# Performance work log

Hardware: AMD Instinct MI355X
Metric: run time of the kernel (lower is better)

## Reference

```python
import jax, jax.numpy as jnp
import numpy as np

D_MODEL = 1024
N_HEADS = 16
D_HEAD = D_MODEL // N_HEADS
D_FF = 4096
EPS = 1e-5


def _layernorm(x, g, b):
    mu = jnp.mean(x, axis=-1, keepdims=True)
    var = jnp.mean(jnp.square(x - mu), axis=-1, keepdims=True)
    return (x - mu) * jax.lax.rsqrt(var + EPS) * g + b


def setup_inputs() -> dict:
    key = jax.random.key(0)
    ks = jax.random.split(key, 16)
    B, S, D = 2, 2048, D_MODEL

    def xavier(k, shape):
        fan_in, fan_out = shape[0], shape[1]
        lim = float(np.sqrt(6.0 / (fan_in + fan_out)))
        return jax.random.uniform(k, shape, jnp.float32, -lim, lim)

    return {
        "x": jax.random.normal(ks[0], (B, S, D), jnp.float32),
        "ln1_g": jnp.ones((D,), jnp.float32),
        "ln1_b": jnp.zeros((D,), jnp.float32),
        "wq": xavier(ks[1], (D, D)), "bq": jnp.zeros((D,), jnp.float32),
        "wk": xavier(ks[2], (D, D)), "bk": jnp.zeros((D,), jnp.float32),
        "wv": xavier(ks[3], (D, D)), "bv": jnp.zeros((D,), jnp.float32),
        "wo": xavier(ks[4], (D, D)), "bo": jnp.zeros((D,), jnp.float32),
        "wf": xavier(ks[5], (D, N_HEADS)), "bf": jnp.zeros((N_HEADS,), jnp.float32),
        "ln2_g": jnp.ones((D,), jnp.float32),
        "ln2_b": jnp.zeros((D,), jnp.float32),
        "w1": xavier(ks[6], (D, D_FF)), "b1": jnp.zeros((D_FF,), jnp.float32),
        "w2": xavier(ks[7], (D_FF, D)), "b2": jnp.zeros((D,), jnp.float32),
    }


def reference(x, ln1_g, ln1_b, wq, bq, wk, bk, wv, bv, wo, bo, wf, bf,
              ln2_g, ln2_b, w1, b1, w2, b2):
    B, S, D = x.shape
    H, Dh = N_HEADS, D_HEAD

    # --- pre-norm forgetting attention ---
    h = _layernorm(x, ln1_g, ln1_b)
    q = (h @ wq + bq).reshape(B, S, H, Dh)
    k = (h @ wk + bk).reshape(B, S, H, Dh)
    v = (h @ wv + bv).reshape(B, S, H, Dh)

    # per-head scalar forget gate f_t in (0,1); cumulative log-decay c_t
    logf = jax.nn.log_sigmoid(h @ wf + bf)           # (B, S, H)
    c = jnp.cumsum(logf, axis=1)                     # (B, S, H)

    scale = 1.0 / jnp.sqrt(jnp.asarray(Dh, x.dtype))
    logits = jnp.einsum("bihd,bjhd->bhij", q, k) * scale
    # decay bias D_ij = c_i - c_j (sum of log forget gates in (j, i])
    decay = c.transpose(0, 2, 1)                     # (B, H, S)
    logits = logits + decay[:, :, :, None] - decay[:, :, None, :]

    causal = jnp.tril(jnp.ones((S, S), bool))
    logits = jnp.where(causal[None, None], logits, -jnp.inf)

    attn = jax.nn.softmax(logits, axis=-1)           # (B, H, S, S)
    ctx = jnp.einsum("bhij,bjhd->bihd", attn, v).reshape(B, S, D)
    attn_out = ctx @ wo + bo

    x = x + attn_out                                 # dropout = identity (eval)

    # --- pre-norm GELU MLP ---
    h2 = _layernorm(x, ln2_g, ln2_b)
    ff = jax.nn.gelu(h2 @ w1 + b1, approximate=False) @ w2 + b2
    return x + ff
```

## Files before the change

kernel.cpp:

```cpp
#include <hip/hip_runtime.h>
#include <hip/hip_bf16.h>
#include <math.h>

typedef unsigned short u16;
typedef unsigned int u32;
typedef __bf16 bf16x8 __attribute__((ext_vector_type(8)));
typedef float f32x4 __attribute__((ext_vector_type(4)));
typedef u32 u32x4 __attribute__((ext_vector_type(4)));

__device__ __forceinline__ u16 f2bf(float f) {
  __hip_bfloat16 h = __float2bfloat16(f);
  return *reinterpret_cast<u16*>(&h);
}
__device__ __forceinline__ float bf2f(u16 u) {
  return __uint_as_float(((u32)u) << 16);
}

#define GLL(gp, lp)                                                     \
  __builtin_amdgcn_global_load_lds(                                     \
      (const __attribute__((address_space(1))) void*)(gp),              \
      (__attribute__((address_space(3))) void*)(lp), 16, 0, 0)

__global__ __launch_bounds__(256) void transpose_cast(
    const float* __restrict__ in, u16* __restrict__ out, int R, int C) {
  __shared__ float tile[32][33];
  int c0 = blockIdx.x * 32, r0 = blockIdx.y * 32;
  int tx = threadIdx.x & 31, ty = threadIdx.x >> 5;
  for (int i = ty; i < 32; i += 8) {
    int r = r0 + i, c = c0 + tx;
    if (r < R && c < C) tile[i][tx] = in[(size_t)r * C + c];
  }
  __syncthreads();
  for (int i = ty; i < 32; i += 8) {
    int c = c0 + i, r = r0 + tx;
    if (c < C && r < R) out[(size_t)c * R + r] = f2bf(tile[tx][i]);
  }
}

__global__ __launch_bounds__(256) void transpose_cast3(
    const float* __restrict__ in0, const float* __restrict__ in1,
    const float* __restrict__ in2, u16* __restrict__ out) {
  __shared__ float tile[32][33];
  const float* in = (blockIdx.z == 0) ? in0 : (blockIdx.z == 1) ? in1 : in2;
  u16* o = out + (size_t)blockIdx.z * 1024 * 1024;
  int c0 = blockIdx.x * 32, r0 = blockIdx.y * 32;
  int tx = threadIdx.x & 31, ty = threadIdx.x >> 5;
  for (int i = ty; i < 32; i += 8)
    tile[i][tx] = in[(size_t)(r0 + i) * 1024 + c0 + tx];
  __syncthreads();
  for (int i = ty; i < 32; i += 8)
    o[(size_t)(c0 + i) * 1024 + r0 + tx] = f2bf(tile[tx][i]);
}

__global__ __launch_bounds__(256) void pack3(
    const float* __restrict__ a, const float* __restrict__ b,
    const float* __restrict__ c, float* __restrict__ o, u32* __restrict__ ctr) {
  int t = blockIdx.x * 256 + threadIdx.x;
  if (t == 0) *ctr = 0u;
  if (t < 1024) o[t] = a[t];
  else if (t < 2048) o[t] = b[t - 1024];
  else if (t < 3072) o[t] = c[t - 2048];
}

__global__ __launch_bounds__(256) void ln_kernel(
    const float* x, const float* __restrict__ g,
    const float* __restrict__ bb, u16* __restrict__ out,
    float* xadd, const float* addb) {
  __shared__ float red[8];
  const int row = blockIdx.x;
  const float* xr = x + (size_t)row * 1024;
  f32x4 v = *(const f32x4*)(xr + threadIdx.x * 4);
  float s = v[0] + v[1] + v[2] + v[3];
  #pragma unroll
  for (int off = 32; off > 0; off >>= 1) s += __shfl_xor(s, off, 64);
  if ((threadIdx.x & 63) == 0) red[threadIdx.x >> 6] = s;
  __syncthreads();
  float mu = (red[0] + red[1] + red[2] + red[3]) * (1.0f / 1024.0f);
  f32x4 d;
  d[0] = v[0] - mu; d[1] = v[1] - mu; d[2] = v[2] - mu; d[3] = v[3] - mu;
  float sq = d[0]*d[0] + d[1]*d[1] + d[2]*d[2] + d[3]*d[3];
  #pragma unroll
  for (int off = 32; off > 0; off >>= 1) sq += __shfl_xor(sq, off, 64);
  if ((threadIdx.x & 63) == 0) red[4 + (threadIdx.x >> 6)] = sq;
  __syncthreads();
  float var = (red[4] + red[5] + red[6] + red[7]) * (1.0f / 1024.0f);
  float rstd = rsqrtf(var + 1e-5f);
  int cb = threadIdx.x * 4;
  #pragma unroll
  for (int e = 0; e < 4; ++e)
    out[(size_t)row * 1024 + cb + e] = f2bf(d[e] * rstd * g[cb + e] + bb[cb + e]);
  if (xadd) {
    f32x4 w;
    #pragma unroll
    for (int e = 0; e < 4; ++e) w[e] = v[e] + addb[cb + e];
    *(f32x4*)(xadd + (size_t)row * 1024 + cb) = w;
  }
}

__global__ __launch_bounds__(256) void gemm_bt(
    const u16* __restrict__ A, const u16* __restrict__ Bt,
    const float* __restrict__ bias, const float* __restrict__ res,
    void* __restrict__ outp, int M, int N, int K, int mode) {
  __shared__ u16 As[128 * 32];
  __shared__ u16 Bs[128 * 32];
  const int tid = threadIdx.x;
  const int m0 = blockIdx.y * 128, n0 = blockIdx.x * 128;
  const int wave = tid >> 6, lane = tid & 63;
  const int wm = (wave >> 1) * 64, wn = (wave & 1) * 64;
  const int lr = lane & 15, quad = lane >> 4;
  const int g0 = wave * 2;
  const int srow0 = g0 * 16 + (lane >> 2);
  const int scol = (lane & 3) * 8;
  const u16* Ag0 = A + (size_t)(m0 + srow0) * K + scol;
  const u16* Ag1 = A + (size_t)(m0 + srow0 + 16) * K + scol;
  const u16* Bg0 = Bt + (size_t)(n0 + srow0) * K + scol;
  const u16* Bg1 = Bt + (size_t)(n0 + srow0 + 16) * K + scol;
  u16* Al0 = As + g0 * 512;
  u16* Al1 = As + (g0 + 1) * 512;
  u16* Bl0 = Bs + g0 * 512;
  u16* Bl1 = Bs + (g0 + 1) * 512;

  f32x4 acc[4][4] = {};

  for (int k0 = 0; k0 < K; k0 += 32) {
    GLL(Ag0 + k0, Al0);
    GLL(Ag1 + k0, Al1);
    GLL(Bg0 + k0, Bl0);
    GLL(Bg1 + k0, Bl1);
    __syncthreads();
    bf16x8 af[4], bfr[4];
    #pragma unroll
    for (int t = 0; t < 4; ++t) {
      af[t]  = *(const bf16x8*)&As[(wm + t * 16 + lr) * 32 + quad * 8];
      bfr[t] = *(const bf16x8*)&Bs[(wn + t * 16 + lr) * 32 + quad * 8];
    }
    #pragma unroll
    for (int mt = 0; mt < 4; ++mt)
      #pragma unroll
      for (int nt = 0; nt < 4; ++nt)
        acc[mt][nt] = __builtin_amdgcn_mfma_f32_16x16x32_bf16(
            af[mt], bfr[nt], acc[mt][nt], 0, 0, 0);
    __syncthreads();
  }

  #pragma unroll
  for (int mt = 0; mt < 4; ++mt) {
    #pragma unroll
    for (int nt = 0; nt < 4; ++nt) {
      const int col = n0 + wn + nt * 16 + lr;
      const float bvv = bias[col];
      #pragma unroll
      for (int rr = 0; rr < 4; ++rr) {
        const int row = m0 + wm + mt * 16 + quad * 4 + rr;
        const size_t idx = (size_t)row * N + col;
        float v = acc[mt][nt][rr] + bvv;
        if (mode == 0) {
          ((float*)outp)[idx] = v;
        } else if (mode == 1) {
          ((float*)outp)[idx] = v + res[idx];
        } else if (mode == 2) {
          float gl = 0.5f * v * (1.0f + erff(v * 0.70710678118654752f));
          ((u16*)outp)[idx] = f2bf(gl);
        } else {
          ((u16*)outp)[idx] = f2bf(v);
        }
      }
    }
  }
}

__global__ __launch_bounds__(256) void gemm_bt_sk(
    const u16* __restrict__ A, const u16* __restrict__ Bt,
    float* __restrict__ outp, int M, int N, int Ktot, int Kslice) {
  __shared__ u16 As[128 * 32];
  __shared__ u16 Bs[128 * 32];
  const int tid = threadIdx.x;
  const int m0 = blockIdx.y * 128, n0 = blockIdx.x * 128;
  const int kbeg = blockIdx.z * Kslice, kend = kbeg + Kslice;
  const int wave = tid >> 6, lane = tid & 63;
  const int wm = (wave >> 1) * 64, wn = (wave & 1) * 64;
  const int lr = lane & 15, quad = lane >> 4;
  const int g0 = wave * 2;
  const int srow0 = g0 * 16 + (lane >> 2);
  const int scol = (lane & 3) * 8;
  const u16* Ag0 = A + (size_t)(m0 + srow0) * Ktot + scol;
  const u16* Ag1 = A + (size_t)(m0 + srow0 + 16) * Ktot + scol;
  const u16* Bg0 = Bt + (size_t)(n0 + srow0) * Ktot + scol;
  const u16* Bg1 = Bt + (size_t)(n0 + srow0 + 16) * Ktot + scol;
  u16* Al0 = As + g0 * 512;
  u16* Al1 = As + (g0 + 1) * 512;
  u16* Bl0 = Bs + g0 * 512;
  u16* Bl1 = Bs + (g0 + 1) * 512;

  f32x4 acc[4][4] = {};

  for (int k0 = kbeg; k0 < kend; k0 += 32) {
    GLL(Ag0 + k0, Al0);
    GLL(Ag1 + k0, Al1);
    GLL(Bg0 + k0, Bl0);
    GLL(Bg1 + k0, Bl1);
    __syncthreads();
    bf16x8 af[4], bfr[4];
    #pragma unroll
    for (int t = 0; t < 4; ++t) {
      af[t]  = *(const bf16x8*)&As[(wm + t * 16 + lr) * 32 + quad * 8];
      bfr[t] = *(const bf16x8*)&Bs[(wn + t * 16 + lr) * 32 + quad * 8];
    }
    #pragma unroll
    for (int mt = 0; mt < 4; ++mt)
      #pragma unroll
      for (int nt = 0; nt < 4; ++nt)
        acc[mt][nt] = __builtin_amdgcn_mfma_f32_16x16x32_bf16(
            af[mt], bfr[nt], acc[mt][nt], 0, 0, 0);
    __syncthreads();
  }

  #pragma unroll
  for (int mt = 0; mt < 4; ++mt) {
    #pragma unroll
    for (int nt = 0; nt < 4; ++nt) {
      const int col = n0 + wn + nt * 16 + lr;
      #pragma unroll
      for (int rr = 0; rr < 4; ++rr) {
        const int row = m0 + wm + mt * 16 + quad * 4 + rr;
        __hip_atomic_fetch_add(&outp[(size_t)row * N + col], acc[mt][nt][rr],
                               __ATOMIC_RELAXED, __HIP_MEMORY_SCOPE_AGENT);
      }
    }
  }
}

__global__ __launch_bounds__(256) void gemm_n64(
    const u16* __restrict__ A, const u16* __restrict__ Bt,
    const float* __restrict__ bias, const float* __restrict__ res,
    void* __restrict__ outp, int M, int N, int K, int mode) {
  __shared__ u16 As[128 * 32];
  __shared__ u16 Bs[64 * 32];
  const int tid = threadIdx.x;
  const int m0 = blockIdx.y * 128, n0 = blockIdx.x * 64;
  const int wave = tid >> 6, lane = tid & 63;
  const int wm = (wave >> 1) * 64, wn = (wave & 1) * 32;
  const int lr = lane & 15, quad = lane >> 4;
  const int g0 = wave * 2;
  const int srow = lane >> 2;
  const int scol = (lane & 3) * 8;
  const u16* Ag0 = A + (size_t)(m0 + g0 * 16 + srow) * K + scol;
  const u16* Ag1 = A + (size_t)(m0 + g0 * 16 + 16 + srow) * K + scol;
  const u16* Bg  = Bt + (size_t)(n0 + wave * 16 + srow) * K + scol;
  u16* Al0 = As + g0 * 512;
  u16* Al1 = As + (g0 + 1) * 512;
  u16* Bl  = Bs + wave * 512;

  f32x4 acc[4][2] = {};

  for (int k0 = 0; k0 < K; k0 += 32) {
    GLL(Ag0 + k0, Al0);
    GLL(Ag1 + k0, Al1);
    GLL(Bg + k0, Bl);
    __syncthreads();
    bf16x8 af[4], bfr[2];
    #pragma unroll
    for (int t = 0; t < 4; ++t)
      af[t] = *(const bf16x8*)&As[(wm + t * 16 + lr) * 32 + quad * 8];
    #pragma unroll
    for (int t = 0; t < 2; ++t)
      bfr[t] = *(const bf16x8*)&Bs[(wn + t * 16 + lr) * 32 + quad * 8];
    #pragma unroll
    for (int mt = 0; mt < 4; ++mt)
      #pragma unroll
      for (int nt = 0; nt < 2; ++nt)
        acc[mt][nt] = __builtin_amdgcn_mfma_f32_16x16x32_bf16(
            af[mt], bfr[nt], acc[mt][nt], 0, 0, 0);
    __syncthreads();
  }

  #pragma unroll
  for (int mt = 0; mt < 4; ++mt) {
    #pragma unroll
    for (int nt = 0; nt < 2; ++nt) {
      const int col = n0 + wn + nt * 16 + lr;
      const float bvv = bias[col];
      #pragma unroll
      for (int rr = 0; rr < 4; ++rr) {
        const int row = m0 + wm + mt * 16 + quad * 4 + rr;
        const size_t idx = (size_t)row * N + col;
        float v = acc[mt][nt][rr] + bvv;
        if (mode == 0) {
          ((float*)outp)[idx] = v;
        } else if (mode == 1) {
          ((float*)outp)[idx] = v + res[idx];
        } else if (mode == 2) {
          float gl = 0.5f * v * (1.0f + erff(v * 0.70710678118654752f));
          ((u16*)outp)[idx] = f2bf(gl);
        } else {
          ((u16*)outp)[idx] = f2bf(v);
        }
      }
    }
  }
}

__global__ __launch_bounds__(64) void logf_kernel(
    const u16* __restrict__ h, const u16* __restrict__ wfT,
    const float* __restrict__ bfv, float* __restrict__ c) {
  const int row = blockIdx.x;
  const int lane = threadIdx.x;
  float acc[16];
  #pragma unroll
  for (int n = 0; n < 16; ++n) acc[n] = 0.f;
  for (int t = 0; t < 16; ++t) {
    int kidx = t * 64 + lane;
    float hv = bf2f(h[(size_t)row * 1024 + kidx]);
    #pragma unroll
    for (int n = 0; n < 16; ++n)
      acc[n] += hv * bf2f(wfT[n * 1024 + kidx]);
  }
  float z = 0.f;
  #pragma unroll
  for (int n = 0; n < 16; ++n) {
    float r = acc[n];
    #pragma unroll
    for (int off = 1; off < 64; off <<= 1) r += __shfl_xor(r, off, 64);
    if (lane == n) z = r;
  }
  if (lane < 16) {
    z += bfv[lane];
    float lf = (z >= 0.f) ? -log1pf(expf(-z)) : (z - log1pf(expf(z)));
    c[(size_t)row * 16 + lane] = lf;
  }
}

__global__ __launch_bounds__(64) void cumsum_kernel(float* __restrict__ c, int S) {
  const int b = blockIdx.x >> 4, h = blockIdx.x & 15;
  const int lane = threadIdx.x;
  float carry = 0.f;
  for (int s0 = 0; s0 < S; s0 += 64) {
    float v = c[(size_t)(b * S + s0 + lane) * 16 + h];
    #pragma unroll
    for (int off = 1; off < 64; off <<= 1) {
      float t = __shfl_up(v, off, 64);
      if (lane >= off) v += t;
    }
    v += carry;
    c[(size_t)(b * S + s0 + lane) * 16 + h] = v;
    carry = __shfl(v, 63, 64);
  }
}

__global__ __launch_bounds__(256) void vtrans(
    const u16* __restrict__ qkvb, u16* __restrict__ vtg) {
  __shared__ u16 t[32][33];
  const int bh = blockIdx.z, b = bh >> 4, h = bh & 15;
  const int s0 = blockIdx.x * 32, d0 = blockIdx.y * 32;
  const int tx = threadIdx.x & 31, ty = threadIdx.x >> 5;
  for (int i = ty; i < 32; i += 8)
    t[i][tx] = qkvb[(size_t)(b * 2048 + s0 + i) * 3072 + 2048 + h * 64 + d0 + tx];
  __syncthreads();
  for (int i = ty; i < 32; i += 8)
    vtg[(size_t)(bh * 64 + d0 + i) * 2048 + s0 + tx] = t[tx][i];
}

__global__ __launch_bounds__(64) void qk_norms(
    const u16* __restrict__ qkvb, float* __restrict__ qkmax) {
  const int tile = blockIdx.x, bh = blockIdx.y, z = blockIdx.z;
  const int b = bh >> 4, h = bh & 15;
  const int tok = tile * 64 + (int)threadIdx.x;
  const u16* p = qkvb + (size_t)(b * 2048 + tok) * 3072 + z * 1024 + h * 64;
  float s = 0.f;
  #pragma unroll
  for (int i = 0; i < 4; ++i) {
    u32x4 w = *(const u32x4*)(p + i * 16);
    u32x4 w2 = *(const u32x4*)(p + i * 16 + 8);
    #pragma unroll
    for (int e = 0; e < 4; ++e) {
      float lo = __uint_as_float(w[e] << 16);
      float hi = __uint_as_float(w[e] & 0xffff0000u);
      float lo2 = __uint_as_float(w2[e] << 16);
      float hi2 = __uint_as_float(w2[e] & 0xffff0000u);
      s += lo * lo + hi * hi + lo2 * lo2 + hi2 * hi2;
    }
  }
  s = sqrtf(s);
  #pragma unroll
  for (int off = 1; off < 64; off <<= 1) s = fmaxf(s, __shfl_xor(s, off, 64));
  if (threadIdx.x == 0) qkmax[z * 1024 + bh * 32 + tile] = s;
}

#define FS 72
#define NITEMS 1024
#define L2E 1.4426950408889634f

__global__ __launch_bounds__(256) void fattn(
    const u16* __restrict__ qkvb, const u16* __restrict__ vtg,
    const float* __restrict__ c, const float* __restrict__ qkmax,
    u16* __restrict__ ctx, u32* __restrict__ ctr) {
  __shared__ u16 Qs[64 * FS];
  __shared__ u16 Ks[64 * FS];
  __shared__ u16 Vt[64 * FS];
  __shared__ u16 Ps[64 * FS];
  __shared__ float cjs[64];
  __shared__ float wmn[4];
  __shared__ u32 sh_item;
  const int S = 2048;
  const int tid = threadIdx.x, wave = tid >> 6, lane = tid & 63;
  const int lr = lane & 15, quad = lane >> 4;
  const int w16 = wave * 16;
  const int sr = tid >> 2, scc = (tid & 3) * 16;

  for (;;) {
    if (tid == 0) sh_item = atomicAdd(ctr, 1u);
    __syncthreads();
    const u32 item = sh_item;
    if (item >= NITEMS) return;
    const int qt = 31 - (int)(item >> 5);
    const int bh = (int)(item & 31), b = bh >> 4, h = bh & 15;
    const int i0 = qt * 64;

    {
      const u16* src = qkvb + (size_t)(b * S + i0 + sr) * 3072 + h * 64 + scc;
      *(u32x4*)&Qs[sr * FS + scc] = *(const u32x4*)src;
      *(u32x4*)&Qs[sr * FS + scc + 8] = *(const u32x4*)(src + 8);
    }
    u32x4 kr0, kr1, vr0, vr1;
    float cjr = 0.f;
    {
      const u16* ks = qkvb + (size_t)(b * S + i0 + sr) * 3072 + 1024 + h * 64 + scc;
      kr0 = *(const u32x4*)ks;
      kr1 = *(const u32x4*)(ks + 8);
      const u16* vs = vtg + (size_t)(bh * 64 + sr) * 2048 + i0 + scc;
      vr0 = *(const u32x4*)vs;
      vr1 = *(const u32x4*)(vs + 8);
      if (tid < 64) cjr = c[(size_t)(b * S + i0 + tid) * 16 + h];
    }
    float bscale;
    {
      float qm = qkmax[bh * 32 + qt];
      float km = 0.f;
      for (int t = 0; t <= qt; ++t) km = fmaxf(km, qkmax[1024 + bh * 32 + t]);
      bscale = qm * km * (0.125f * L2E);
    }
    float m_[4], l_[4], alpha[4];
    f32x4 o_[4];
    #pragma unroll
    for (int r = 0; r < 4; ++r) {
      m_[r] = -INFINITY;
      l_[r] = 0.f;
    }
    #pragma unroll
    for (int dt = 0; dt < 4; ++dt) o_[dt] = (f32x4){0.f, 0.f, 0.f, 0.f};

    __syncthreads();
    const bf16x8 aq0 = *(const bf16x8*)&Qs[(w16 + lr) * FS + quad * 8];
    const bf16x8 aq1 = *(const bf16x8*)&Qs[(w16 + lr) * FS + 32 + quad * 8];

    for (int jt = qt; jt >= 0; --jt) {
      const int j0 = jt * 64;
      *(u32x4*)&Ks[sr * FS + scc] = kr0;
      *(u32x4*)&Ks[sr * FS + scc + 8] = kr1;
      *(u32x4*)&Vt[sr * FS + scc] = vr0;
      *(u32x4*)&Vt[sr * FS + scc + 8] = vr1;
      if (tid < 64) cjs[tid] = cjr * L2E;
      if (jt > 0) {
        const int j1 = j0 - 64;
        const u16* ks = qkvb + (size_t)(b * S + j1 + sr) * 3072 + 1024 + h * 64 + scc;
        kr0 = *(const u32x4*)ks;
        kr1 = *(const u32x4*)(ks + 8);
        const u16* vs = vtg + (size_t)(bh * 64 + sr) * 2048 + j1 + scc;
        vr0 = *(const u32x4*)vs;
        vr1 = *(const u32x4*)(vs + 8);
        if (tid < 64) cjr = c[(size_t)(b * S + j1 + tid) * 16 + h];
      }
      __syncthreads();

      f32x4 sc[4];
      #pragma unroll
      for (int nt = 0; nt < 4; ++nt) {
        bf16x8 bk0 = *(const bf16x8*)&Ks[(nt * 16 + lr) * FS + quad * 8];
        bf16x8 bk1 = *(const bf16x8*)&Ks[(nt * 16 + lr) * FS + 32 + quad * 8];
        f32x4 z = {0.f, 0.f, 0.f, 0.f};
        z = __builtin_amdgcn_mfma_f32_16x16x32_bf16(aq0, bk0, z, 0, 0, 0);
        z = __builtin_amdgcn_mfma_f32_16x16x32_bf16(aq1, bk1, z, 0, 0, 0);
        sc[nt] = z;
      }
      const bool diag = (jt == qt);
      #pragma unroll
      for (int r = 0; r < 4; ++r) {
        const int i = i0 + w16 + quad * 4 + r;
        float lg[4], mrow = -INFINITY;
        #pragma unroll
        for (int nt = 0; nt < 4; ++nt) {
          const int j = j0 + nt * 16 + lr;
          float v = sc[nt][r] * (0.125f * L2E) - cjs[nt * 16 + lr];
          if (diag && (j > i)) v = -INFINITY;
          lg[nt] = v;
          mrow = fmaxf(mrow, v);
        }
        #pragma unroll
        for (int off = 1; off < 16; off <<= 1)
          mrow = fmaxf(mrow, __shfl_xor(mrow, off, 64));
        const float mn = fmaxf(m_[r], mrow);
        alpha[r] = __builtin_exp2f(m_[r] - mn);
        m_[r] = mn;
        float rs = 0.f;
        #pragma unroll
        for (int nt = 0; nt < 4; ++nt) {
          const float p = __builtin_exp2f(lg[nt] - mn);
          Ps[(w16 + quad * 4 + r) * FS + nt * 16 + lr] = f2bf(p);
          rs += p;
        }
        l_[r] = l_[r] * alpha[r] + rs;
      }
      asm volatile("s_waitcnt lgkmcnt(0)" ::: "memory");
      #pragma unroll
      for (int dt = 0; dt < 4; ++dt)
        #pragma unroll
        for (int r = 0; r < 4; ++r) o_[dt][r] *= alpha[r];
      bf16x8 ap0 = *(const bf16x8*)&Ps[(w16 + lr) * FS + quad * 8];
      bf16x8 ap1 = *(const bf16x8*)&Ps[(w16 + lr) * FS + 32 + quad * 8];
      #pragma unroll
      for (int dt = 0; dt < 4; ++dt) {
        bf16x8 bv0 = *(const bf16x8*)&Vt[(dt * 16 + lr) * FS + quad * 8];
        bf16x8 bv1 = *(const bf16x8*)&Vt[(dt * 16 + lr) * FS + 32 + quad * 8];
        o_[dt] = __builtin_amdgcn_mfma_f32_16x16x32_bf16(ap0, bv0, o_[dt], 0, 0, 0);
        o_[dt] = __builtin_amdgcn_mfma_f32_16x16x32_bf16(ap1, bv1, o_[dt], 0, 0, 0);
      }
      {
        float wmin = fminf(fminf(m_[0], m_[1]), fminf(m_[2], m_[3]));
        wmin = fminf(wmin, __shfl_xor(wmin, 16, 64));
        wmin = fminf(wmin, __shfl_xor(wmin, 32, 64));
        if (lane == 0) wmn[wave] = wmin;
      }
      __syncthreads();
      if (jt > 0) {
        const float bmin = fminf(fminf(wmn[0], wmn[1]), fminf(wmn[2], wmn[3]));
        const float cend = c[(size_t)(b * S + j0 - 1) * 16 + h];
        if (bscale - cend * L2E < bmin - 40.f) break;
      }
    }
    #pragma unroll
    for (int r = 0; r < 4; ++r) {
      float lt = l_[r];
      #pragma unroll
      for (int off = 1; off < 16; off <<= 1) lt += __shfl_xor(lt, off, 64);
      const float inv = 1.0f / lt;
      const size_t base = (size_t)(b * S + i0 + w16 + quad * 4 + r) * 1024 + h * 64;
      #pragma unroll
      for (int dt = 0; dt < 4; ++dt)
        ctx[base + dt * 16 + lr] = f2bf(o_[dt][r] * inv);
    }
  }
}

extern "C" void kernel_launch(void* const* d_in, const int* in_sizes, int n_in,
                              void* d_out, int out_size, void* d_ws, size_t ws_size,
                              hipStream_t stream) {
  const float* x    = (const float*)d_in[0];
  const float* ln1g = (const float*)d_in[1];
  const float* ln1b = (const float*)d_in[2];
  const float* wq   = (const float*)d_in[3];
  const float* bq   = (const float*)d_in[4];
  const float* wk   = (const float*)d_in[5];
  const float* bk   = (const float*)d_in[6];
  const float* wv   = (const float*)d_in[7];
  const float* bv   = (const float*)d_in[8];
  const float* wo   = (const float*)d_in[9];
  const float* bo   = (const float*)d_in[10];
  const float* wf   = (const float*)d_in[11];
  const float* bfv  = (const float*)d_in[12];
  const float* ln2g = (const float*)d_in[13];
  const float* ln2b = (const float*)d_in[14];
  const float* w1   = (const float*)d_in[15];
  const float* b1   = (const float*)d_in[16];
  const float* w2   = (const float*)d_in[17];
  const float* b2   = (const float*)d_in[18];
  float* out = (float*)d_out;

  char* ws = (char*)d_ws;
  const size_t MB = 1024 * 1024;
  u16*   wqkvT = (u16*)(ws + 0 * MB);
  u16*   woT   = (u16*)(ws + 6 * MB);
  u16*   w1T   = (u16*)(ws + 8 * MB);
  u16*   w2T   = (u16*)(ws + 16 * MB);
  u16*   wfT   = (u16*)(ws + 24 * MB);
  float* bqkv  = (float*)(ws + 24 * MB + 65536);
  u32*   fctr  = (u32*)(ws + 24 * MB + 131072);
  u16*   hbuf  = (u16*)(ws + 25 * MB);
  u16*   ctx   = (u16*)(ws + 33 * MB);
  u16*   qkvb  = (u16*)(ws + 41 * MB);
  u16*   vtg   = (u16*)(ws + 65 * MB);
  float* cb    = (float*)(ws + 73 * MB);
  float* qkmax = (float*)(ws + 73 * MB + 262144);
  u16*   act1  = (u16*)(ws + 74 * MB);

  dim3 blk(256);
  transpose_cast3<<<dim3(32, 32, 3), blk, 0, stream>>>(wq, wk, wv, wqkvT);
  transpose_cast<<<dim3(32, 32), blk, 0, stream>>>(wo, woT, 1024, 1024);
  transpose_cast<<<dim3(128, 32), blk, 0, stream>>>(w1, w1T, 1024, 4096);
  transpose_cast<<<dim3(32, 128), blk, 0, stream>>>(w2, w2T, 4096, 1024);
  transpose_cast<<<dim3(1, 32), blk, 0, stream>>>(wf, wfT, 1024, 16);
  pack3<<<12, blk, 0, stream>>>(bq, bk, bv, bqkv, fctr);
  ln_kernel<<<4096, blk, 0, stream>>>(x, ln1g, ln1b, hbuf, nullptr, nullptr);
  gemm_bt<<<dim3(24, 32), blk, 0, stream>>>(hbuf, wqkvT, bqkv, nullptr, qkvb,
                                            4096, 3072, 1024, 3);
  logf_kernel<<<4096, dim3(64), 0, stream>>>(hbuf, wfT, bfv, cb);
  cumsum_kernel<<<32, dim3(64), 0, stream>>>(cb, 2048);
  vtrans<<<dim3(64, 2, 32), blk, 0, stream>>>(qkvb, vtg);
  qk_norms<<<dim3(32, 32, 2), dim3(64), 0, stream>>>(qkvb, qkmax);
  fattn<<<dim3(1024), blk, 0, stream>>>(qkvb, vtg, cb, qkmax, ctx, fctr);
  gemm_n64<<<dim3(16, 32), blk, 0, stream>>>(ctx, woT, bo, x, out,
                                             4096, 1024, 1024, 1);
  ln_kernel<<<4096, blk, 0, stream>>>(out, ln2g, ln2b, hbuf, out, b2);
  gemm_bt<<<dim3(32, 32), blk, 0, stream>>>(hbuf, w1T, b1, nullptr, act1,
                                            4096, 4096, 1024, 2);
  gemm_bt_sk<<<dim3(8, 32, 4), blk, 0, stream>>>(act1, w2T, out,
                                                 4096, 1024, 4096, 1024);
}
```

Before: 501.2 us.

## Double-buffer LDS tiles in GEMM kernels to overlap global loads with MFMA

Adds a second shared-memory buffer to the three bf16 GEMM kernels and issues the global-to-LDS loads for the next K-step before computing on the current one. The aim is to hide global memory latency behind MFMA work instead of stalling on a barrier right after each load. It doubles LDS use per block, which could reduce occupancy. It also relies on a single barrier per iteration to cover both the async loads and the buffer reuse.

```diff
diff --git a/kernel.cpp b/kernel.cpp
--- a/kernel.cpp
+++ b/kernel.cpp
@@ -101,8 +101,8 @@
     const u16* __restrict__ A, const u16* __restrict__ Bt,
     const float* __restrict__ bias, const float* __restrict__ res,
     void* __restrict__ outp, int M, int N, int K, int mode) {
-  __shared__ u16 As[128 * 32];
-  __shared__ u16 Bs[128 * 32];
+  __shared__ u16 As[2 * 128 * 32];
+  __shared__ u16 Bs[2 * 128 * 32];
   const int tid = threadIdx.x;
   const int m0 = blockIdx.y * 128, n0 = blockIdx.x * 128;
   const int wave = tid >> 6, lane = tid & 63;
@@ -115,24 +115,30 @@
   const u16* Ag1 = A + (size_t)(m0 + srow0 + 16) * K + scol;
   const u16* Bg0 = Bt + (size_t)(n0 + srow0) * K + scol;
   const u16* Bg1 = Bt + (size_t)(n0 + srow0 + 16) * K + scol;
-  u16* Al0 = As + g0 * 512;
-  u16* Al1 = As + (g0 + 1) * 512;
-  u16* Bl0 = Bs + g0 * 512;
-  u16* Bl1 = Bs + (g0 + 1) * 512;
+  const int ao0 = g0 * 512, ao1 = (g0 + 1) * 512;
 
   f32x4 acc[4][4] = {};
 
+  GLL(Ag0, As + ao0);
+  GLL(Ag1, As + ao1);
+  GLL(Bg0, Bs + ao0);
+  GLL(Bg1, Bs + ao1);
+  __syncthreads();
+
+  int cur = 0;
   for (int k0 = 0; k0 < K; k0 += 32) {
-    GLL(Ag0 + k0, Al0);
-    GLL(Ag1 + k0, Al1);
-    GLL(Bg0 + k0, Bl0);
-    GLL(Bg1 + k0, Bl1);
-    __syncthreads();
+    const int cb = cur * 4096, nb = (cur ^ 1) * 4096;
+    if (k0 + 32 < K) {
+      GLL(Ag0 + k0 + 32, As + nb + ao0);
+      GLL(Ag1 + k0 + 32, As + nb + ao1);
+      GLL(Bg0 + k0 + 32, Bs + nb + ao0);
+      GLL(Bg1 + k0 + 32, Bs + nb + ao1);
+    }
     bf16x8 af[4], bfr[4];
     #pragma unroll
     for (int t = 0; t < 4; ++t) {
-      af[t]  = *(const bf16x8*)&As[(wm + t * 16 + lr) * 32 + quad * 8];
-      bfr[t] = *(const bf16x8*)&Bs[(wn + t * 16 + lr) * 32 + quad * 8];
+      af[t]  = *(const bf16x8*)&As[cb + (wm + t * 16 + lr) * 32 + quad * 8];
+      bfr[t] = *(const bf16x8*)&Bs[cb + (wn + t * 16 + lr) * 32 + quad * 8];
     }
     #pragma unroll
     for (int mt = 0; mt < 4; ++mt)
@@ -141,6 +147,7 @@
         acc[mt][nt] = __builtin_amdgcn_mfma_f32_16x16x32_bf16(
             af[mt], bfr[nt], acc[mt][nt], 0, 0, 0);
     __syncthreads();
+    cur ^= 1;
   }
 
   #pragma unroll
@@ -172,8 +179,8 @@
 __global__ __launch_bounds__(256) void gemm_bt_sk(
     const u16* __restrict__ A, const u16* __restrict__ Bt,
     float* __restrict__ outp, int M, int N, int Ktot, int Kslice) {
-  __shared__ u16 As[128 * 32];
-  __shared__ u16 Bs[128 * 32];
+  __shared__ u16 As[2 * 128 * 32];
+  __shared__ u16 Bs[2 * 128 * 32];
   const int tid = threadIdx.x;
   const int m0 = blockIdx.y * 128, n0 = blockIdx.x * 128;
   const int kbeg = blockIdx.z * Kslice, kend = kbeg + Kslice;
@@ -187,24 +194,30 @@
   const u16* Ag1 = A + (size_t)(m0 + srow0 + 16) * Ktot + scol;
   const u16* Bg0 = Bt + (size_t)(n0 + srow0) * Ktot + scol;
   const u16* Bg1 = Bt + (size_t)(n0 + srow0 + 16) * Ktot + scol;
-  u16* Al0 = As + g0 * 512;
-  u16* Al1 = As + (g0 + 1) * 512;
-  u16* Bl0 = Bs + g0 * 512;
-  u16* Bl1 = Bs + (g0 + 1) * 512;
+  const int ao0 = g0 * 512, ao1 = (g0 + 1) * 512;
 
   f32x4 acc[4][4] = {};
 
+  GLL(Ag0 + kbeg, As + ao0);
+  GLL(Ag1 + kbeg, As + ao1);
+  GLL(Bg0 + kbeg, Bs + ao0);
+  GLL(Bg1 + kbeg, Bs + ao1);
+  __syncthreads();
+
+  int cur = 0;
   for (int k0 = kbeg; k0 < kend; k0 += 32) {
-    GLL(Ag0 + k0, Al0);
-    GLL(Ag1 + k0, Al1);
-    GLL(Bg0 + k0, Bl0);
-    GLL(Bg1 + k0, Bl1);
-    __syncthreads();
+    const int cb = cur * 4096, nb = (cur ^ 1) * 4096;
+    if (k0 + 32 < kend) {
+      GLL(Ag0 + k0 + 32, As + nb + ao0);
+      GLL(Ag1 + k0 + 32, As + nb + ao1);
+      GLL(Bg0 + k0 + 32, Bs + nb + ao0);
+      GLL(Bg1 + k0 + 32, Bs + nb + ao1);
+    }
     bf16x8 af[4], bfr[4];
     #pragma unroll
     for (int t = 0; t < 4; ++t) {
-      af[t]  = *(const bf16x8*)&As[(wm + t * 16 + lr) * 32 + quad * 8];
-      bfr[t] = *(const bf16x8*)&Bs[(wn + t * 16 + lr) * 32 + quad * 8];
+      af[t]  = *(const bf16x8*)&As[cb + (wm + t * 16 + lr) * 32 + quad * 8];
+      bfr[t] = *(const bf16x8*)&Bs[cb + (wn + t * 16 + lr) * 32 + quad * 8];
     }
     #pragma unroll
     for (int mt = 0; mt < 4; ++mt)
@@ -213,6 +226,7 @@
         acc[mt][nt] = __builtin_amdgcn_mfma_f32_16x16x32_bf16(
             af[mt], bfr[nt], acc[mt][nt], 0, 0, 0);
     __syncthreads();
+    cur ^= 1;
   }
 
   #pragma unroll
@@ -234,8 +248,8 @@
     const u16* __restrict__ A, const u16* __restrict__ Bt,
     const float* __restrict__ bias, const float* __restrict__ res,
     void* __restrict__ outp, int M, int N, int K, int mode) {
-  __shared__ u16 As[128 * 32];
-  __shared__ u16 Bs[64 * 32];
+  __shared__ u16 As[2 * 128 * 32];
+  __shared__ u16 Bs[2 * 64 * 32];
   const int tid = threadIdx.x;
   const int m0 = blockIdx.y * 128, n0 = blockIdx.x * 64;
   const int wave = tid >> 6, lane = tid & 63;
@@ -247,24 +261,31 @@
   const u16* Ag0 = A + (size_t)(m0 + g0 * 16 + srow) * K + scol;
   const u16* Ag1 = A + (size_t)(m0 + g0 * 16 + 16 + srow) * K + scol;
   const u16* Bg  = Bt + (size_t)(n0 + wave * 16 + srow) * K + scol;
-  u16* Al0 = As + g0 * 512;
-  u16* Al1 = As + (g0 + 1) * 512;
-  u16* Bl  = Bs + wave * 512;
+  const int ao0 = g0 * 512, ao1 = (g0 + 1) * 512, bo = wave * 512;
 
   f32x4 acc[4][2] = {};
 
+  GLL(Ag0, As + ao0);
+  GLL(Ag1, As + ao1);
+  GLL(Bg, Bs + bo);
+  __syncthreads();
+
+  int cur = 0;
   for (int k0 = 0; k0 < K; k0 += 32) {
-    GLL(Ag0 + k0, Al0);
-    GLL(Ag1 + k0, Al1);
-    GLL(Bg + k0, Bl);
-    __syncthreads();
+    const int cba = cur * 4096, nba = (cur ^ 1) * 4096;
+    const int cbb = cur * 2048, nbb = (cur ^ 1) * 2048;
+    if (k0 + 32 < K) {
+      GLL(Ag0 + k0 + 32, As + nba + ao0);
+      GLL(Ag1 + k0 + 32, As + nba + ao1);
+      GLL(Bg + k0 + 32, Bs + nbb + bo);
+    }
     bf16x8 af[4], bfr[2];
     #pragma unroll
     for (int t = 0; t < 4; ++t)
-      af[t] = *(const bf16x8*)&As[(wm + t * 16 + lr) * 32 + quad * 8];
+      af[t] = *(const bf16x8*)&As[cba + (wm + t * 16 + lr) * 32 + quad * 8];
     #pragma unroll
     for (int t = 0; t < 2; ++t)
-      bfr[t] = *(const bf16x8*)&Bs[(wn + t * 16 + lr) * 32 + quad * 8];
+      bfr[t] = *(const bf16x8*)&Bs[cbb + (wn + t * 16 + lr) * 32 + quad * 8];
     #pragma unroll
     for (int mt = 0; mt < 4; ++mt)
       #pragma unroll
@@ -272,6 +293,7 @@
         acc[mt][nt] = __builtin_amdgcn_mfma_f32_16x16x32_bf16(
             af[mt], bfr[nt], acc[mt][nt], 0, 0, 0);
     __syncthreads();
+    cur ^= 1;
   }
 
   #pragma unroll
```

New measurement: 481.1 us. 1.04x faster.
